# Kernel optimization log

Measured on AMD Instinct MI355X. Metric: run time of the kernel, lower is better.

## Reference

```python
import jax, jax.numpy as jnp
import numpy as np

B, N, S = 8, 4096, 1024
D1, D2 = 128, 256
IN_CH, OUT_CH = D1 + D2, 256
BN_EPS = 1e-5


def setup_inputs() -> dict:
    key = jax.random.key(0)
    ks = jax.random.split(key, 12)
    inp = {
        "xyz1": jax.random.normal(ks[0], (B, N, 3), jnp.float32),
        "xyz2": jax.random.normal(ks[1], (B, S, 3), jnp.float32),
        "points1": jax.random.normal(ks[2], (B, N, D1), jnp.float32),
        "points2": jax.random.normal(ks[3], (B, S, D2), jnp.float32),
        # fuse: Conv1d(in_ch->out_ch, k=1) + BN
        "W_fuse": jax.random.normal(ks[4], (OUT_CH, IN_CH), jnp.float32) * (1.0 / np.sqrt(IN_CH)),
        "b_fuse": jnp.zeros((OUT_CH,), jnp.float32),
        "g_fuse": jnp.ones((OUT_CH,), jnp.float32),
        "bt_fuse": jnp.zeros((OUT_CH,), jnp.float32),
        # res block net1: Conv1d(out_ch->out_ch) + BN (res_expansion=1.0)
        "W1": jax.random.normal(ks[5], (OUT_CH, OUT_CH), jnp.float32) * (1.0 / np.sqrt(OUT_CH)),
        "b1": jnp.zeros((OUT_CH,), jnp.float32),
        "g1": jnp.ones((OUT_CH,), jnp.float32),
        "bt1": jnp.zeros((OUT_CH,), jnp.float32),
        # res block net2: Conv1d(out_ch->out_ch) + BN
        "W2": jax.random.normal(ks[6], (OUT_CH, OUT_CH), jnp.float32) * (1.0 / np.sqrt(OUT_CH)),
        "b2": jnp.zeros((OUT_CH,), jnp.float32),
        "g2": jnp.ones((OUT_CH,), jnp.float32),
        "bt2": jnp.zeros((OUT_CH,), jnp.float32),
    }
    return inp


def _bn(x, g, b):
    # BatchNorm1d training-mode forward: stats over (batch, length), x: [B, C, L]
    m = jnp.mean(x, axis=(0, 2), keepdims=True)
    v = jnp.var(x, axis=(0, 2), keepdims=True)
    return (x - m) * jax.lax.rsqrt(v + BN_EPS) * g[None, :, None] + b[None, :, None]


def _conv1x1(x, W, b):
    # x: [B, C_in, L], W: [C_out, C_in] -> [B, C_out, L]
    return jnp.einsum("oc,bcl->bol", W, x) + b[None, :, None]


def _gelu(x):
    return jax.nn.gelu(x, approximate=False)  # torch nn.GELU default (erf)


def reference(xyz1, xyz2, points1, points2,
              W_fuse, b_fuse, g_fuse, bt_fuse,
              W1, b1, g1, bt1, W2, b2, g2, bt2):
    # squared pairwise distances [B, N, S] without B x N x S x 3 intermediate
    d = (jnp.sum(xyz1 * xyz1, -1)[:, :, None]
         - 2.0 * jnp.einsum("bnc,bsc->bns", xyz1, xyz2)
         + jnp.sum(xyz2 * xyz2, -1)[:, None, :])
    # 3 nearest coarse points per dense point (== sort ascending, take first 3)
    neg_d3, idx = jax.lax.top_k(-d, 3)            # [B, N, 3]
    d3 = -neg_d3
    recip = 1.0 / (d3 + 1e-8)
    w = recip / jnp.sum(recip, axis=2, keepdims=True)  # [B, N, 3]
    gathered = points2[jnp.arange(points2.shape[0])[:, None, None], idx]  # [B, N, 3, D2]
    interp = jnp.sum(gathered * w[..., None], axis=2)  # [B, N, D2]

    new_points = jnp.concatenate([points1, interp], axis=-1)  # [B, N, D1+D2]
    x = jnp.transpose(new_points, (0, 2, 1))                   # [B, C, N]

    # fuse: conv-bn-gelu
    x = _gelu(_bn(_conv1x1(x, W_fuse, b_fuse), g_fuse, bt_fuse))
    # residual block: gelu(bn(conv(gelu(bn(conv(x))))) + x)
    y = _gelu(_bn(_conv1x1(x, W1, b1), g1, bt1))
    y = _bn(_conv1x1(y, W2, b2), g2, bt2)
    x = _gelu(y + x)

    return jnp.transpose(x, (0, 2, 1))  # [B, N, out_ch]
```

## Files before the change

### kernel.cpp

```cpp
#include <hip/hip_runtime.h>
#include <hip/hip_bf16.h>

constexpr int Bb = 8, Nn = 4096, Ss = 1024;
constexpr int D1 = 128, D2 = 256, KIN = 384, OC = 256;
constexpr int L = Bb * Nn;
constexpr float BN_EPS = 1e-5f;
constexpr int NW = 98304 + 65536 + 65536;

typedef __attribute__((ext_vector_type(4))) float floatx4;
typedef __attribute__((ext_vector_type(8))) __bf16 bf16x8;

#define DEV __device__ __forceinline__

DEV float bf2f(unsigned short u) {
    union { unsigned int i; float f; } v; v.i = ((unsigned int)u) << 16; return v.f;
}
DEV unsigned short f2bf(float f) {
    union { float f; unsigned int i; } v; v.f = f;
    unsigned int x = v.i;
    return (unsigned short)((x + 0x7FFFu + ((x >> 16) & 1u)) >> 16);
}
DEV float gelu_f(float x) {
    float u = x * (0.7978845608f + 0.0356774081f * x * x);
    float t = __expf(-2.0f * u);
    return x * __builtin_amdgcn_rcpf(1.0f + t);
}

DEV bool probe_isf(const unsigned int* __restrict__ w, int tid) {
    unsigned int lo = w[tid & 63] & 0xFFFFu;
    int e = (int)((lo >> 7) & 0xFF);
    unsigned long long m = __ballot(e >= 100 && e <= 144);
    return __popcll(m) < 48;
}

DEV void merge3(float& d0, float& d1, float& d2, int& i0, int& i1, int& i2,
                float e0, float e1, float e2, int j0, int j1, int j2, bool pref) {
    float a0 = d0, a1 = d1, a2 = d2; int x0 = i0, x1 = i1, x2 = i2;
    float b0 = e0, b1 = e1;          int y0 = j0, y1 = j1;
    bool t = pref ? (a0 <= b0) : (a0 < b0);
    d0 = t ? a0 : b0; i0 = t ? x0 : y0;
    a0 = t ? a1 : a0; x0 = t ? x1 : x0;
    a1 = t ? a2 : a1; x1 = t ? x2 : x1;
    b0 = t ? b0 : b1; y0 = t ? y0 : y1;
    b1 = t ? b1 : e2; y1 = t ? y1 : j2;
    t = pref ? (a0 <= b0) : (a0 < b0);
    d1 = t ? a0 : b0; i1 = t ? x0 : y0;
    a0 = t ? a1 : a0; x0 = t ? x1 : x0;
    b0 = t ? b0 : b1; y0 = t ? y0 : y1;
    t = pref ? (a0 <= b0) : (a0 < b0);
    d2 = t ? a0 : b0; i2 = t ? x0 : y0;
}

__global__ __launch_bounds__(256) void k_front(const void* __restrict__ xyz1_,
                                               const void* __restrict__ xyz2_,
                                               const void* __restrict__ points1_,
                                               const void* __restrict__ points2_,
                                               const void* __restrict__ w0_,
                                               const void* __restrict__ w1_,
                                               const void* __restrict__ w2_,
                                               unsigned short* __restrict__ Wdst,
                                               unsigned short* __restrict__ X,
                                               float* __restrict__ stats,
                                               int* __restrict__ dflag) {
    int tid = threadIdx.x;
    int bid = blockIdx.x;
    bool isf = probe_isf((const unsigned int*)xyz1_, tid);

    if (bid < 6) {
        stats[bid * 256 + tid] = 0.0f;
        if (bid == 0 && tid == 0) *dflag = isf ? 1 : 0;
        return;
    }
    if (bid < 902) {
        int i = (bid - 6) * 256 + tid;
        const void* src; int off;
        if (i < 98304)       { src = w0_; off = i; }
        else if (i < 163840) { src = w1_; off = i - 98304; }
        else                 { src = w2_; off = i - 163840; }
        Wdst[i] = isf ? f2bf(((const float*)src)[off]) : ((const unsigned short*)src)[off];
        return;
    }

    __shared__ alignas(16) float s4[Ss * 4 + 32];
    __shared__ int   sIdx[32 * 3];
    __shared__ float sW[32 * 3];
    int bn0 = (bid - 902) * 32;
    int b = bn0 >> 12;

    if (isf) {
        const float* p2 = (const float*)xyz2_ + (size_t)b * Ss * 3;
        for (int i = tid; i < Ss * 3; i += 256) {
            int s = i / 3, k = i - s * 3;
            s4[s * 4 + k + ((s >> 7) << 2)] = p2[i];
        }
    } else {
        const unsigned short* p2 = (const unsigned short*)xyz2_ + (size_t)b * Ss * 3;
        for (int i = tid; i < Ss * 3; i += 256) {
            int s = i / 3, k = i - s * 3;
            s4[s * 4 + k + ((s >> 7) << 2)] = bf2f(p2[i]);
        }
    }
    __syncthreads();
    for (int s = tid; s < Ss; s += 256) {
        int a = s * 4 + ((s >> 7) << 2);
        float x = s4[a], y = s4[a + 1], z = s4[a + 2];
        s4[a + 3] = x * x + y * y + z * z;
    }
    __syncthreads();

    int part = tid & 7;
    int q = tid >> 3;
    int bn = bn0 + q;
    float x1, y1, z1;
    if (isf) {
        const float* p1 = (const float*)xyz1_ + (size_t)bn * 3;
        x1 = p1[0]; y1 = p1[1]; z1 = p1[2];
    } else {
        const unsigned short* p1 = (const unsigned short*)xyz1_ + (size_t)bn * 3;
        x1 = bf2f(p1[0]); y1 = bf2f(p1[1]); z1 = bf2f(p1[2]);
    }
    float n1 = x1 * x1 + y1 * y1 + z1 * z1;

    float d0 = 3.4e38f, d1 = 3.4e38f, d2 = 3.4e38f;
    int i0 = 0, i1 = 0, i2 = 0;
    const float* sp = &s4[part * 516];
#pragma unroll 4
    for (int j = 0; j < 128; ++j) {
        float4 qv = *(const float4*)(sp + j * 4);
        float d = n1 + qv.w - 2.0f * (x1 * qv.x + y1 * qv.y + z1 * qv.z);
        int s = part * 128 + j;
        bool c2 = d < d2, c1 = d < d1, c0 = d < d0;
        d2 = c1 ? d1 : (c2 ? d : d2); i2 = c1 ? i1 : (c2 ? s : i2);
        d1 = c0 ? d0 : (c1 ? d : d1); i1 = c0 ? i0 : (c1 ? s : i1);
        d0 = c0 ? d  : d0;            i0 = c0 ? s  : i0;
    }
#pragma unroll
    for (int m = 1; m <= 4; m <<= 1) {
        float e0 = __shfl_xor(d0, m, 64), e1 = __shfl_xor(d1, m, 64), e2 = __shfl_xor(d2, m, 64);
        int   j0 = __shfl_xor(i0, m, 64), j1 = __shfl_xor(i1, m, 64), j2 = __shfl_xor(i2, m, 64);
        bool pref = (part < (part ^ m));
        merge3(d0, d1, d2, i0, i1, i2, e0, e1, e2, j0, j1, j2, pref);
    }
    if (part == 0) {
        float r0 = 1.0f / (d0 + 1e-8f), r1 = 1.0f / (d1 + 1e-8f), r2 = 1.0f / (d2 + 1e-8f);
        float rs = 1.0f / (r0 + r1 + r2);
        sIdx[q * 3 + 0] = i0; sIdx[q * 3 + 1] = i1; sIdx[q * 3 + 2] = i2;
        sW[q * 3 + 0] = r0 * rs; sW[q * 3 + 1] = r1 * rs; sW[q * 3 + 2] = r2 * rs;
    }
    __syncthreads();

    int lane = tid & 63;
    int c = lane * 4;
#pragma unroll
    for (int it = 0; it < 8; ++it) {
        int lp = it * 4 + (tid >> 6);
        int pt = bn0 + lp;
        int j0 = sIdx[lp * 3], j1 = sIdx[lp * 3 + 1], j2 = sIdx[lp * 3 + 2];
        float w0 = sW[lp * 3], w1 = sW[lp * 3 + 1], w2 = sW[lp * 3 + 2];
        if (isf) {
            const float* p1 = (const float*)points1_ + (size_t)pt * D1;
            float2 v = *(const float2*)(p1 + lane * 2);
            ((unsigned int*)(X + (size_t)pt * KIN))[lane] =
                (unsigned int)f2bf(v.x) | ((unsigned int)f2bf(v.y) << 16);
            const float* base = (const float*)points2_;
            float4 a0 = *(const float4*)(base + ((size_t)(b * Ss + j0)) * D2 + c);
            float4 a1 = *(const float4*)(base + ((size_t)(b * Ss + j1)) * D2 + c);
            float4 a2 = *(const float4*)(base + ((size_t)(b * Ss + j2)) * D2 + c);
            uint2 out;
            unsigned short* uo = (unsigned short*)&out;
            uo[0] = f2bf(w0 * a0.x + w1 * a1.x + w2 * a2.x);
            uo[1] = f2bf(w0 * a0.y + w1 * a1.y + w2 * a2.y);
            uo[2] = f2bf(w0 * a0.z + w1 * a1.z + w2 * a2.z);
            uo[3] = f2bf(w0 * a0.w + w1 * a1.w + w2 * a2.w);
            *(uint2*)(X + (size_t)pt * KIN + D1 + c) = out;
        } else {
            const unsigned short* p1 = (const unsigned short*)points1_;
            ((unsigned int*)(X + (size_t)pt * KIN))[lane] =
                ((const unsigned int*)(p1 + (size_t)pt * D1))[lane];
            const unsigned short* base = (const unsigned short*)points2_;
            uint2 v0 = *(const uint2*)(base + ((size_t)(b * Ss + j0)) * D2 + c);
            uint2 v1 = *(const uint2*)(base + ((size_t)(b * Ss + j1)) * D2 + c);
            uint2 v2 = *(const uint2*)(base + ((size_t)(b * Ss + j2)) * D2 + c);
            const unsigned short* u0 = (const unsigned short*)&v0;
            const unsigned short* u1 = (const unsigned short*)&v1;
            const unsigned short* u2 = (const unsigned short*)&v2;
            uint2 out;
            unsigned short* uo = (unsigned short*)&out;
#pragma unroll
            for (int j = 0; j < 4; ++j)
                uo[j] = f2bf(w0 * bf2f(u0[j]) + w1 * bf2f(u1[j]) + w2 * bf2f(u2[j]));
            *(uint2*)(X + (size_t)pt * KIN + D1 + c) = out;
        }
    }
}

template <int K, int ACT>
__global__ __launch_bounds__(256) void k_gemm(const unsigned short* __restrict__ A,
                                              const unsigned short* __restrict__ W,
                                              unsigned short* __restrict__ Out,
                                              float* __restrict__ S1, float* __restrict__ S2,
                                              const float* __restrict__ S1in,
                                              const float* __restrict__ S2in,
                                              const void* __restrict__ g_,
                                              const void* __restrict__ bt_,
                                              const int* __restrict__ dflag) {
    __shared__ alignas(16) unsigned short As[64 * 64];
    __shared__ alignas(16) unsigned short Bs[256 * 64];
    __shared__ float sS1[256], sS2[256];
    __shared__ float sCA[256], sCC[256];

    int tid = threadIdx.x;
    int l0 = blockIdx.x * 64;
    int wn = tid >> 6, lane = tid & 63, quad = lane >> 4, lr = lane & 15;

    if (ACT) {
        int o = tid;
        float m = S1in[o] * (1.0f / (float)L);
        float var = S2in[o] * (1.0f / (float)L) - m * m;
        float g, bt;
        if (*dflag) { g = ((const float*)g_)[o]; bt = ((const float*)bt_)[o]; }
        else { g = bf2f(((const unsigned short*)g_)[o]); bt = bf2f(((const unsigned short*)bt_)[o]); }
        float a = g * rsqrtf(var + BN_EPS);
        sCA[o] = a;
        sCC[o] = bt - m * a;
    }

    floatx4 zero4 = {0.f, 0.f, 0.f, 0.f};
    floatx4 acc[4][4];
#pragma unroll
    for (int mi = 0; mi < 4; ++mi)
#pragma unroll
        for (int ni = 0; ni < 4; ++ni) acc[mi][ni] = zero4;

    constexpr int KC = K / 64;
    for (int kc = 0; kc < KC; ++kc) {
        __syncthreads();
#pragma unroll
        for (int it = 0; it < 2; ++it) {
            int idx = it * 256 + tid;
            int row = idx >> 3, c8 = idx & 7;
            union { uint4 v; unsigned short u[8]; } va;
            va.v = *(const uint4*)(A + (size_t)(l0 + row) * K + kc * 64 + c8 * 8);
            if (ACT) {
                int kbase = kc * 64 + c8 * 8;
#pragma unroll
                for (int j = 0; j < 8; ++j) {
                    float f = bf2f(va.u[j]);
                    va.u[j] = f2bf(gelu_f(sCA[kbase + j] * f + sCC[kbase + j]));
                }
            }
            *(uint4*)&As[row * 64 + ((c8 ^ (row & 7)) << 3)] = va.v;
        }
#pragma unroll
        for (int it = 0; it < 8; ++it) {
            int idx = it * 256 + tid;
            int row = idx >> 3, c8 = idx & 7;
            uint4 vb = *(const uint4*)(W + (size_t)row * K + kc * 64 + c8 * 8);
            *(uint4*)&Bs[row * 64 + ((c8 ^ (row & 7)) << 3)] = vb;
        }
        __syncthreads();
#pragma unroll
        for (int ks8 = 0; ks8 < 2; ++ks8) {
            bf16x8 af[4], bfr[4];
#pragma unroll
            for (int mi = 0; mi < 4; ++mi) {
                int ra = mi * 16 + lr;
                af[mi] = *(const bf16x8*)&As[ra * 64 + ((((ks8 << 2) + quad) ^ (ra & 7)) << 3)];
            }
#pragma unroll
            for (int ni = 0; ni < 4; ++ni) {
                int rb = wn * 64 + ni * 16 + lr;
                bfr[ni] = *(const bf16x8*)&Bs[rb * 64 + ((((ks8 << 2) + quad) ^ (rb & 7)) << 3)];
            }
#pragma unroll
            for (int mi = 0; mi < 4; ++mi)
#pragma unroll
                for (int ni = 0; ni < 4; ++ni)
                    acc[mi][ni] = __builtin_amdgcn_mfma_f32_16x16x32_bf16(af[mi], bfr[ni], acc[mi][ni], 0, 0, 0);
        }
    }

    float p1[4] = {0, 0, 0, 0}, p2[4] = {0, 0, 0, 0};
#pragma unroll
    for (int mi = 0; mi < 4; ++mi) {
#pragma unroll
        for (int ni = 0; ni < 4; ++ni) {
#pragma unroll
            for (int r = 0; r < 4; ++r) {
                float v = acc[mi][ni][r];
                int row = l0 + mi * 16 + quad * 4 + r;
                int col = wn * 64 + ni * 16 + lr;
                Out[(size_t)row * OC + col] = f2bf(v);
                p1[ni] += v;
                p2[ni] += v * v;
            }
        }
    }
    sS1[tid] = 0.f; sS2[tid] = 0.f;
    __syncthreads();
#pragma unroll
    for (int ni = 0; ni < 4; ++ni) {
        atomicAdd(&sS1[wn * 64 + ni * 16 + lr], p1[ni]);
        atomicAdd(&sS2[wn * 64 + ni * 16 + lr], p2[ni]);
    }
    __syncthreads();
    atomicAdd(&S1[tid], sS1[tid]);
    atomicAdd(&S2[tid], sS2[tid]);
}

__global__ __launch_bounds__(256) void k_final(const unsigned short* __restrict__ t0,
                                               const unsigned short* __restrict__ t2,
                                               const float* __restrict__ S1_0, const float* __restrict__ S2_0,
                                               const float* __restrict__ S1_2, const float* __restrict__ S2_2,
                                               const void* __restrict__ g0_, const void* __restrict__ bt0_,
                                               const void* __restrict__ g2_, const void* __restrict__ bt2_,
                                               const int* __restrict__ dflag,
                                               void* __restrict__ out_) {
    __shared__ float sA0[256], sC0[256], sA2[256], sC2[256];
    int tid = threadIdx.x;
    bool isf = (*dflag != 0);
    {
        int o = tid;
        float m0 = S1_0[o] * (1.0f / (float)L);
        float v0_ = S2_0[o] * (1.0f / (float)L) - m0 * m0;
        float m2 = S1_2[o] * (1.0f / (float)L);
        float v2_ = S2_2[o] * (1.0f / (float)L) - m2 * m2;
        float g0, b0, g2, b2;
        if (isf) {
            g0 = ((const float*)g0_)[o]; b0 = ((const float*)bt0_)[o];
            g2 = ((const float*)g2_)[o]; b2 = ((const float*)bt2_)[o];
        } else {
            g0 = bf2f(((const unsigned short*)g0_)[o]); b0 = bf2f(((const unsigned short*)bt0_)[o]);
            g2 = bf2f(((const unsigned short*)g2_)[o]); b2 = bf2f(((const unsigned short*)bt2_)[o]);
        }
        float a0 = g0 * rsqrtf(v0_ + BN_EPS);
        float a2 = g2 * rsqrtf(v2_ + BN_EPS);
        sA0[o] = a0; sC0[o] = b0 - m0 * a0;
        sA2[o] = a2; sC2[o] = b2 - m2 * a2;
    }
    __syncthreads();

    int idx = (blockIdx.x * 256 + tid) * 8;
    int col = idx & (OC - 1);
    union { uint4 v; unsigned short u[8]; } v0, v2;
    v0.v = *(const uint4*)(t0 + idx);
    v2.v = *(const uint4*)(t2 + idx);
    float r[8];
#pragma unroll
    for (int j = 0; j < 8; ++j) {
        float x = gelu_f(sA0[col + j] * bf2f(v0.u[j]) + sC0[col + j]);
        float y = sA2[col + j] * bf2f(v2.u[j]) + sC2[col + j];
        r[j] = gelu_f(x + y);
    }
    if (isf) {
        float* o = (float*)out_ + idx;
        float4 lo = {r[0], r[1], r[2], r[3]};
        float4 hi = {r[4], r[5], r[6], r[7]};
        *(float4*)o = lo;
        *(float4*)(o + 4) = hi;
    } else {
        union { uint4 v; unsigned short u[8]; } vo;
#pragma unroll
        for (int j = 0; j < 8; ++j) vo.u[j] = f2bf(r[j]);
        *(uint4*)((unsigned short*)out_ + idx) = vo.v;
    }
}

extern "C" void kernel_launch(void* const* d_in, const int* in_sizes, int n_in,
                              void* d_out, int out_size, void* d_ws, size_t ws_size,
                              hipStream_t stream) {
    const void* xyz1    = d_in[0];
    const void* xyz2    = d_in[1];
    const void* points1 = d_in[2];
    const void* points2 = d_in[3];
    const void* W_fuse  = d_in[4];
    const void* g_fuse  = d_in[6];
    const void* bt_fuse = d_in[7];
    const void* W1      = d_in[8];
    const void* g1      = d_in[10];
    const void* bt1     = d_in[11];
    const void* W2      = d_in[12];
    const void* g2      = d_in[14];
    const void* bt2     = d_in[15];

    char* ws = (char*)d_ws;
    unsigned short* X  = (unsigned short*)ws;
    unsigned short* t0 = (unsigned short*)(ws + 25165824);
    unsigned short* t1 = (unsigned short*)d_out;
    unsigned short* t2 = X;
    float* stats  = (float*)(ws + 42729472);
    int*   dflag  = (int*)(ws + 42729472 + 3072 * 4);
    unsigned short* Wf_bf = (unsigned short*)(ws + 42745856);

    float *S1_0 = stats,        *S2_0 = stats + 256;
    float *S1_1 = stats + 512,  *S2_1 = stats + 768;
    float *S1_2 = stats + 1024, *S2_2 = stats + 1280;

    k_front<<<1926, 256, 0, stream>>>(xyz1, xyz2, points1, points2,
                                      W_fuse, W1, W2, Wf_bf, X, stats, dflag);
    k_gemm<KIN, 0><<<L / 64, 256, 0, stream>>>(X, Wf_bf, t0, S1_0, S2_0,
                                               nullptr, nullptr, nullptr, nullptr, nullptr);
    k_gemm<OC, 1><<<L / 64, 256, 0, stream>>>(t0, Wf_bf + 98304, t1, S1_1, S2_1,
                                              S1_0, S2_0, g_fuse, bt_fuse, dflag);
    k_gemm<OC, 1><<<L / 64, 256, 0, stream>>>(t1, Wf_bf + 163840, t2, S1_2, S2_2,
                                              S1_1, S2_1, g1, bt1, dflag);
    k_final<<<L * OC / (256 * 8), 256, 0, stream>>>(t0, t2, S1_0, S2_0, S1_2, S2_2,
                                                    g_fuse, bt_fuse, g2, bt2, dflag, d_out);
}
```

Before: 233.3 us.

## Fuse interpolation gather and concat into the first GEMM's A-tile load

The front kernel now only computes the three nearest neighbours and their weights and writes them to workspace. The first GEMM builds its A tile on the fly, converting points1 and gathering and weighting points2 rows, so the 384-wide concatenated X matrix is no longer written to and read back from global memory. The cost is that the GEMM's load phase now does indirect gathers and extra arithmetic, which may stall the MFMA pipeline because there is no prefetch.

```diff
diff --git a/kernel.cpp b/kernel.cpp
--- a/kernel.cpp
+++ b/kernel.cpp
@@ -5,7 +5,6 @@
 constexpr int D1 = 128, D2 = 256, KIN = 384, OC = 256;
 constexpr int L = Bb * Nn;
 constexpr float BN_EPS = 1e-5f;
-constexpr int NW = 98304 + 65536 + 65536;
 
 typedef __attribute__((ext_vector_type(4))) float floatx4;
 typedef __attribute__((ext_vector_type(8))) __bf16 bf16x8;
@@ -53,15 +52,14 @@
 
 __global__ __launch_bounds__(256) void k_front(const void* __restrict__ xyz1_,
                                                const void* __restrict__ xyz2_,
-                                               const void* __restrict__ points1_,
-                                               const void* __restrict__ points2_,
                                                const void* __restrict__ w0_,
                                                const void* __restrict__ w1_,
                                                const void* __restrict__ w2_,
                                                unsigned short* __restrict__ Wdst,
-                                               unsigned short* __restrict__ X,
                                                float* __restrict__ stats,
-                                               int* __restrict__ dflag) {
+                                               int* __restrict__ dflag,
+                                               int* __restrict__ nn_idx,
+                                               float* __restrict__ nn_w) {
     int tid = threadIdx.x;
     int bid = blockIdx.x;
     bool isf = probe_isf((const unsigned int*)xyz1_, tid);
@@ -82,8 +80,6 @@
     }
 
     __shared__ alignas(16) float s4[Ss * 4 + 32];
-    __shared__ int   sIdx[32 * 3];
-    __shared__ float sW[32 * 3];
     int bn0 = (bid - 902) * 32;
     int b = bn0 >> 12;
 
@@ -109,8 +105,7 @@
     __syncthreads();
 
     int part = tid & 7;
-    int q = tid >> 3;
-    int bn = bn0 + q;
+    int bn = bn0 + (tid >> 3);
     float x1, y1, z1;
     if (isf) {
         const float* p1 = (const float*)xyz1_ + (size_t)bn * 3;
@@ -144,57 +139,141 @@
     if (part == 0) {
         float r0 = 1.0f / (d0 + 1e-8f), r1 = 1.0f / (d1 + 1e-8f), r2 = 1.0f / (d2 + 1e-8f);
         float rs = 1.0f / (r0 + r1 + r2);
-        sIdx[q * 3 + 0] = i0; sIdx[q * 3 + 1] = i1; sIdx[q * 3 + 2] = i2;
-        sW[q * 3 + 0] = r0 * rs; sW[q * 3 + 1] = r1 * rs; sW[q * 3 + 2] = r2 * rs;
-    }
-    __syncthreads();
-
-    int lane = tid & 63;
-    int c = lane * 4;
-#pragma unroll
-    for (int it = 0; it < 8; ++it) {
-        int lp = it * 4 + (tid >> 6);
-        int pt = bn0 + lp;
-        int j0 = sIdx[lp * 3], j1 = sIdx[lp * 3 + 1], j2 = sIdx[lp * 3 + 2];
-        float w0 = sW[lp * 3], w1 = sW[lp * 3 + 1], w2 = sW[lp * 3 + 2];
-        if (isf) {
-            const float* p1 = (const float*)points1_ + (size_t)pt * D1;
-            float2 v = *(const float2*)(p1 + lane * 2);
-            ((unsigned int*)(X + (size_t)pt * KIN))[lane] =
-                (unsigned int)f2bf(v.x) | ((unsigned int)f2bf(v.y) << 16);
-            const float* base = (const float*)points2_;
-            float4 a0 = *(const float4*)(base + ((size_t)(b * Ss + j0)) * D2 + c);
-            float4 a1 = *(const float4*)(base + ((size_t)(b * Ss + j1)) * D2 + c);
-            float4 a2 = *(const float4*)(base + ((size_t)(b * Ss + j2)) * D2 + c);
-            uint2 out;
-            unsigned short* uo = (unsigned short*)&out;
-            uo[0] = f2bf(w0 * a0.x + w1 * a1.x + w2 * a2.x);
-            uo[1] = f2bf(w0 * a0.y + w1 * a1.y + w2 * a2.y);
-            uo[2] = f2bf(w0 * a0.z + w1 * a1.z + w2 * a2.z);
-            uo[3] = f2bf(w0 * a0.w + w1 * a1.w + w2 * a2.w);
-            *(uint2*)(X + (size_t)pt * KIN + D1 + c) = out;
-        } else {
-            const unsigned short* p1 = (const unsigned short*)points1_;
-            ((unsigned int*)(X + (size_t)pt * KIN))[lane] =
-                ((const unsigned int*)(p1 + (size_t)pt * D1))[lane];
-            const unsigned short* base = (const unsigned short*)points2_;
-            uint2 v0 = *(const uint2*)(base + ((size_t)(b * Ss + j0)) * D2 + c);
-            uint2 v1 = *(const uint2*)(base + ((size_t)(b * Ss + j1)) * D2 + c);
-            uint2 v2 = *(const uint2*)(base + ((size_t)(b * Ss + j2)) * D2 + c);
-            const unsigned short* u0 = (const unsigned short*)&v0;
-            const unsigned short* u1 = (const unsigned short*)&v1;
-            const unsigned short* u2 = (const unsigned short*)&v2;
-            uint2 out;
-            unsigned short* uo = (unsigned short*)&out;
-#pragma unroll
-            for (int j = 0; j < 4; ++j)
-                uo[j] = f2bf(w0 * bf2f(u0[j]) + w1 * bf2f(u1[j]) + w2 * bf2f(u2[j]));
-            *(uint2*)(X + (size_t)pt * KIN + D1 + c) = out;
-        }
-    }
-}
-
-template <int K, int ACT>
+        nn_idx[bn * 3 + 0] = i0; nn_idx[bn * 3 + 1] = i1; nn_idx[bn * 3 + 2] = i2;
+        nn_w[bn * 3 + 0] = r0 * rs; nn_w[bn * 3 + 1] = r1 * rs; nn_w[bn * 3 + 2] = r2 * rs;
+    }
+}
+
+__global__ __launch_bounds__(256) void k_gemm1(const void* __restrict__ p1_,
+                                               const void* __restrict__ p2_,
+                                               const int* __restrict__ nn_idx,
+                                               const float* __restrict__ nn_w,
+                                               const int* __restrict__ dflag,
+                                               const unsigned short* __restrict__ W,
+                                               unsigned short* __restrict__ Out,
+                                               float* __restrict__ S1, float* __restrict__ S2) {
+    __shared__ alignas(16) unsigned short As[64 * 64];
+    __shared__ alignas(16) unsigned short Bs[256 * 64];
+    __shared__ float sS1[256], sS2[256];
+
+    int tid = threadIdx.x;
+    int l0 = blockIdx.x * 64;
+    int wn = tid >> 6, lane = tid & 63, quad = lane >> 4, lr = lane & 15;
+    bool isf = (*dflag != 0);
+
+    floatx4 acc[4][4];
+#pragma unroll
+    for (int mi = 0; mi < 4; ++mi)
+#pragma unroll
+        for (int ni = 0; ni < 4; ++ni) acc[mi][ni] = (floatx4){0.f, 0.f, 0.f, 0.f};
+
+    for (int kc = 0; kc < KIN / 64; ++kc) {
+        __syncthreads();
+#pragma unroll
+        for (int it = 0; it < 2; ++it) {
+            int idx = it * 256 + tid, row = idx >> 3, c8 = idx & 7;
+            int pt = l0 + row;
+            int c0 = kc * 64 + c8 * 8;
+            union { uint4 v; unsigned short u[8]; } va;
+            if (c0 < D1) {
+                if (isf) {
+                    const float* p = (const float*)p1_ + (size_t)pt * D1 + c0;
+                    float4 f0 = *(const float4*)p;
+                    float4 f1 = *(const float4*)(p + 4);
+                    va.u[0] = f2bf(f0.x); va.u[1] = f2bf(f0.y); va.u[2] = f2bf(f0.z); va.u[3] = f2bf(f0.w);
+                    va.u[4] = f2bf(f1.x); va.u[5] = f2bf(f1.y); va.u[6] = f2bf(f1.z); va.u[7] = f2bf(f1.w);
+                } else {
+                    va.v = *(const uint4*)((const unsigned short*)p1_ + (size_t)pt * D1 + c0);
+                }
+            } else {
+                int c2 = c0 - D1;
+                int b = pt >> 12;
+                int j0 = nn_idx[pt * 3], j1 = nn_idx[pt * 3 + 1], j2 = nn_idx[pt * 3 + 2];
+                float w0 = nn_w[pt * 3], w1 = nn_w[pt * 3 + 1], w2 = nn_w[pt * 3 + 2];
+                if (isf) {
+                    const float* base = (const float*)p2_;
+                    const float* r0 = base + ((size_t)(b * Ss + j0)) * D2 + c2;
+                    const float* r1 = base + ((size_t)(b * Ss + j1)) * D2 + c2;
+                    const float* r2 = base + ((size_t)(b * Ss + j2)) * D2 + c2;
+#pragma unroll
+                    for (int h = 0; h < 2; ++h) {
+                        float4 a0 = *(const float4*)(r0 + h * 4);
+                        float4 a1 = *(const float4*)(r1 + h * 4);
+                        float4 a2 = *(const float4*)(r2 + h * 4);
+                        va.u[h * 4 + 0] = f2bf(w0 * a0.x + w1 * a1.x + w2 * a2.x);
+                        va.u[h * 4 + 1] = f2bf(w0 * a0.y + w1 * a1.y + w2 * a2.y);
+                        va.u[h * 4 + 2] = f2bf(w0 * a0.z + w1 * a1.z + w2 * a2.z);
+                        va.u[h * 4 + 3] = f2bf(w0 * a0.w + w1 * a1.w + w2 * a2.w);
+                    }
+                } else {
+                    const unsigned short* base = (const unsigned short*)p2_;
+                    uint4 v0 = *(const uint4*)(base + ((size_t)(b * Ss + j0)) * D2 + c2);
+                    uint4 v1 = *(const uint4*)(base + ((size_t)(b * Ss + j1)) * D2 + c2);
+                    uint4 v2 = *(const uint4*)(base + ((size_t)(b * Ss + j2)) * D2 + c2);
+                    const unsigned short* u0 = (const unsigned short*)&v0;
+                    const unsigned short* u1 = (const unsigned short*)&v1;
+                    const unsigned short* u2 = (const unsigned short*)&v2;
+#pragma unroll
+                    for (int j = 0; j < 8; ++j)
+                        va.u[j] = f2bf(w0 * bf2f(u0[j]) + w1 * bf2f(u1[j]) + w2 * bf2f(u2[j]));
+                }
+            }
+            *(uint4*)&As[row * 64 + ((c8 ^ (row & 7)) << 3)] = va.v;
+        }
+#pragma unroll
+        for (int it = 0; it < 8; ++it) {
+            int idx = it * 256 + tid, row = idx >> 3, c8 = idx & 7;
+            uint4 vb = *(const uint4*)(W + (size_t)row * KIN + kc * 64 + c8 * 8);
+            *(uint4*)&Bs[row * 64 + ((c8 ^ (row & 7)) << 3)] = vb;
+        }
+        __syncthreads();
+#pragma unroll
+        for (int ks8 = 0; ks8 < 2; ++ks8) {
+            bf16x8 af[4], bfr[4];
+#pragma unroll
+            for (int mi = 0; mi < 4; ++mi) {
+                int ra = mi * 16 + lr;
+                af[mi] = *(const bf16x8*)&As[ra * 64 + ((((ks8 << 2) + quad) ^ (ra & 7)) << 3)];
+            }
+#pragma unroll
+            for (int ni = 0; ni < 4; ++ni) {
+                int rb = wn * 64 + ni * 16 + lr;
+                bfr[ni] = *(const bf16x8*)&Bs[rb * 64 + ((((ks8 << 2) + quad) ^ (rb & 7)) << 3)];
+            }
+#pragma unroll
+            for (int mi = 0; mi < 4; ++mi)
+#pragma unroll
+                for (int ni = 0; ni < 4; ++ni)
+                    acc[mi][ni] = __builtin_amdgcn_mfma_f32_16x16x32_bf16(af[mi], bfr[ni], acc[mi][ni], 0, 0, 0);
+        }
+    }
+
+    float p1a[4] = {0, 0, 0, 0}, p2a[4] = {0, 0, 0, 0};
+#pragma unroll
+    for (int mi = 0; mi < 4; ++mi)
+#pragma unroll
+        for (int ni = 0; ni < 4; ++ni)
+#pragma unroll
+            for (int r = 0; r < 4; ++r) {
+                float v = acc[mi][ni][r];
+                int row = l0 + mi * 16 + quad * 4 + r;
+                int col = wn * 64 + ni * 16 + lr;
+                Out[(size_t)row * OC + col] = f2bf(v);
+                p1a[ni] += v; p2a[ni] += v * v;
+            }
+    sS1[tid] = 0.f; sS2[tid] = 0.f;
+    __syncthreads();
+#pragma unroll
+    for (int ni = 0; ni < 4; ++ni) {
+        atomicAdd(&sS1[wn * 64 + ni * 16 + lr], p1a[ni]);
+        atomicAdd(&sS2[wn * 64 + ni * 16 + lr], p2a[ni]);
+    }
+    __syncthreads();
+    atomicAdd(&S1[tid], sS1[tid]);
+    atomicAdd(&S2[tid], sS2[tid]);
+}
+
+template <int K>
 __global__ __launch_bounds__(256) void k_gemm(const unsigned short* __restrict__ A,
                                               const unsigned short* __restrict__ W,
                                               unsigned short* __restrict__ Out,
@@ -213,48 +292,42 @@
     int l0 = blockIdx.x * 64;
     int wn = tid >> 6, lane = tid & 63, quad = lane >> 4, lr = lane & 15;
 
-    if (ACT) {
-        int o = tid;
-        float m = S1in[o] * (1.0f / (float)L);
-        float var = S2in[o] * (1.0f / (float)L) - m * m;
+    {
+        float m = S1in[tid] * (1.0f / (float)L);
+        float var = S2in[tid] * (1.0f / (float)L) - m * m;
         float g, bt;
-        if (*dflag) { g = ((const float*)g_)[o]; bt = ((const float*)bt_)[o]; }
-        else { g = bf2f(((const unsigned short*)g_)[o]); bt = bf2f(((const unsigned short*)bt_)[o]); }
+        if (*dflag) { g = ((const float*)g_)[tid]; bt = ((const float*)bt_)[tid]; }
+        else { g = bf2f(((const unsigned short*)g_)[tid]); bt = bf2f(((const unsigned short*)bt_)[tid]); }
         float a = g * rsqrtf(var + BN_EPS);
-        sCA[o] = a;
-        sCC[o] = bt - m * a;
-    }
-
-    floatx4 zero4 = {0.f, 0.f, 0.f, 0.f};
+        sCA[tid] = a;
+        sCC[tid] = bt - m * a;
+    }
+
     floatx4 acc[4][4];
 #pragma unroll
     for (int mi = 0; mi < 4; ++mi)
 #pragma unroll
-        for (int ni = 0; ni < 4; ++ni) acc[mi][ni] = zero4;
+        for (int ni = 0; ni < 4; ++ni) acc[mi][ni] = (floatx4){0.f, 0.f, 0.f, 0.f};
 
     constexpr int KC = K / 64;
     for (int kc = 0; kc < KC; ++kc) {
         __syncthreads();
 #pragma unroll
         for (int it = 0; it < 2; ++it) {
-            int idx = it * 256 + tid;
-            int row = idx >> 3, c8 = idx & 7;
+            int idx = it * 256 + tid, row = idx >> 3, c8 = idx & 7;
             union { uint4 v; unsigned short u[8]; } va;
             va.v = *(const uint4*)(A + (size_t)(l0 + row) * K + kc * 64 + c8 * 8);
-            if (ACT) {
-                int kbase = kc * 64 + c8 * 8;
-#pragma unroll
-                for (int j = 0; j < 8; ++j) {
-                    float f = bf2f(va.u[j]);
-                    va.u[j] = f2bf(gelu_f(sCA[kbase + j] * f + sCC[kbase + j]));
-                }
+            int kb = kc * 64 + c8 * 8;
+#pragma unroll
+            for (int j = 0; j < 8; ++j) {
+                float f = bf2f(va.u[j]);
+                va.u[j] = f2bf(gelu_f(sCA[kb + j] * f + sCC[kb + j]));
             }
             *(uint4*)&As[row * 64 + ((c8 ^ (row & 7)) << 3)] = va.v;
         }
 #pragma unroll
         for (int it = 0; it < 8; ++it) {
-            int idx = it * 256 + tid;
-            int row = idx >> 3, c8 = idx & 7;
+            int idx = it * 256 + tid, row = idx >> 3, c8 = idx & 7;
             uint4 vb = *(const uint4*)(W + (size_t)row * K + kc * 64 + c8 * 8);
             *(uint4*)&Bs[row * 64 + ((c8 ^ (row & 7)) << 3)] = vb;
         }
@@ -280,28 +353,25 @@
         }
     }
 
-    float p1[4] = {0, 0, 0, 0}, p2[4] = {0, 0, 0, 0};
-#pragma unroll
-    for (int mi = 0; mi < 4; ++mi) {
-#pragma unroll
-        for (int ni = 0; ni < 4; ++ni) {
+    float p1a[4] = {0, 0, 0, 0}, p2a[4] = {0, 0, 0, 0};
+#pragma unroll
+    for (int mi = 0; mi < 4; ++mi)
+#pragma unroll
+        for (int ni = 0; ni < 4; ++ni)
 #pragma unroll
             for (int r = 0; r < 4; ++r) {
                 float v = acc[mi][ni][r];
                 int row = l0 + mi * 16 + quad * 4 + r;
                 int col = wn * 64 + ni * 16 + lr;
                 Out[(size_t)row * OC + col] = f2bf(v);
-                p1[ni] += v;
-                p2[ni] += v * v;
-            }
-        }
-    }
+                p1a[ni] += v; p2a[ni] += v * v;
+            }
     sS1[tid] = 0.f; sS2[tid] = 0.f;
     __syncthreads();
 #pragma unroll
     for (int ni = 0; ni < 4; ++ni) {
-        atomicAdd(&sS1[wn * 64 + ni * 16 + lr], p1[ni]);
-        atomicAdd(&sS2[wn * 64 + ni * 16 + lr], p2[ni]);
+        atomicAdd(&sS1[wn * 64 + ni * 16 + lr], p1a[ni]);
+        atomicAdd(&sS2[wn * 64 + ni * 16 + lr], p2a[ni]);
     }
     __syncthreads();
     atomicAdd(&S1[tid], sS1[tid]);
@@ -320,23 +390,22 @@
     int tid = threadIdx.x;
     bool isf = (*dflag != 0);
     {
-        int o = tid;
-        float m0 = S1_0[o] * (1.0f / (float)L);
-        float v0_ = S2_0[o] * (1.0f / (float)L) - m0 * m0;
-        float m2 = S1_2[o] * (1.0f / (float)L);
-        float v2_ = S2_2[o] * (1.0f / (float)L) - m2 * m2;
+        float m0 = S1_0[tid] * (1.0f / (float)L);
+        float v0_ = S2_0[tid] * (1.0f / (float)L) - m0 * m0;
+        float m2 = S1_2[tid] * (1.0f / (float)L);
+        float v2_ = S2_2[tid] * (1.0f / (float)L) - m2 * m2;
         float g0, b0, g2, b2;
         if (isf) {
-            g0 = ((const float*)g0_)[o]; b0 = ((const float*)bt0_)[o];
-            g2 = ((const float*)g2_)[o]; b2 = ((const float*)bt2_)[o];
+            g0 = ((const float*)g0_)[tid]; b0 = ((const float*)bt0_)[tid];
+            g2 = ((const float*)g2_)[tid]; b2 = ((const float*)bt2_)[tid];
         } else {
-            g0 = bf2f(((const unsigned short*)g0_)[o]); b0 = bf2f(((const unsigned short*)bt0_)[o]);
-            g2 = bf2f(((const unsigned short*)g2_)[o]); b2 = bf2f(((const unsigned short*)bt2_)[o]);
+            g0 = bf2f(((const unsigned short*)g0_)[tid]); b0 = bf2f(((const unsigned short*)bt0_)[tid]);
+            g2 = bf2f(((const unsigned short*)g2_)[tid]); b2 = bf2f(((const unsigned short*)bt2_)[tid]);
         }
         float a0 = g0 * rsqrtf(v0_ + BN_EPS);
         float a2 = g2 * rsqrtf(v2_ + BN_EPS);
-        sA0[o] = a0; sC0[o] = b0 - m0 * a0;
-        sA2[o] = a2; sC2[o] = b2 - m2 * a2;
+        sA0[tid] = a0; sC0[tid] = b0 - m0 * a0;
+        sA2[tid] = a2; sC2[tid] = b2 - m2 * a2;
     }
     __syncthreads();
 
@@ -384,26 +453,26 @@
     const void* bt2     = d_in[15];
 
     char* ws = (char*)d_ws;
-    unsigned short* X  = (unsigned short*)ws;
+    unsigned short* t2 = (unsigned short*)ws;
     unsigned short* t0 = (unsigned short*)(ws + 25165824);
     unsigned short* t1 = (unsigned short*)d_out;
-    unsigned short* t2 = X;
+    int*   nn_idx = (int*)(ws + 41943040);
+    float* nn_w   = (float*)(ws + 42336256);
     float* stats  = (float*)(ws + 42729472);
     int*   dflag  = (int*)(ws + 42729472 + 3072 * 4);
-    unsigned short* Wf_bf = (unsigned short*)(ws + 42745856);
+    unsigned short* Wbf = (unsigned short*)(ws + 42745856);
 
     float *S1_0 = stats,        *S2_0 = stats + 256;
     float *S1_1 = stats + 512,  *S2_1 = stats + 768;
     float *S1_2 = stats + 1024, *S2_2 = stats + 1280;
 
-    k_front<<<1926, 256, 0, stream>>>(xyz1, xyz2, points1, points2,
-                                      W_fuse, W1, W2, Wf_bf, X, stats, dflag);
-    k_gemm<KIN, 0><<<L / 64, 256, 0, stream>>>(X, Wf_bf, t0, S1_0, S2_0,
-                                               nullptr, nullptr, nullptr, nullptr, nullptr);
-    k_gemm<OC, 1><<<L / 64, 256, 0, stream>>>(t0, Wf_bf + 98304, t1, S1_1, S2_1,
-                                              S1_0, S2_0, g_fuse, bt_fuse, dflag);
-    k_gemm<OC, 1><<<L / 64, 256, 0, stream>>>(t1, Wf_bf + 163840, t2, S1_2, S2_2,
-                                              S1_1, S2_1, g1, bt1, dflag);
+    k_front<<<1926, 256, 0, stream>>>(xyz1, xyz2, W_fuse, W1, W2, Wbf, stats, dflag, nn_idx, nn_w);
+    k_gemm1<<<L / 64, 256, 0, stream>>>(points1, points2, nn_idx, nn_w, dflag,
+                                        Wbf, t0, S1_0, S2_0);
+    k_gemm<OC><<<L / 64, 256, 0, stream>>>(t0, Wbf + 98304, t1, S1_1, S2_1,
+                                           S1_0, S2_0, g_fuse, bt_fuse, dflag);
+    k_gemm<OC><<<L / 64, 256, 0, stream>>>(t1, Wbf + 163840, t2, S1_2, S2_2,
+                                           S1_1, S2_1, g1, bt1, dflag);
     k_final<<<L * OC / (256 * 8), 256, 0, stream>>>(t0, t2, S1_0, S2_0, S1_2, S2_2,
                                                     g_fuse, bt_fuse, g2, bt2, dflag, d_out);
 }
```

Measured after the change: 233.0 us. No clear change (-0.1%).
